# Performance work log

Measured on AMD Instinct MI355X. Metric: run time of the kernel, lower is better.

The kernel has to match this reference:

```python
import jax, jax.numpy as jnp
import numpy as np

D = 1024      # n_embd
F = 1024      # moe_inter_dim (ffn_hidden_size)
E = 8         # moe_num_experts
K = 2         # moe_top_k
B, T = 2, 2048


def setup_inputs() -> dict:
    key = jax.random.key(0)
    ks = jax.random.split(key, 7)
    std = 0.02
    x = jax.random.normal(ks[0], (B, T, D), dtype=jnp.float32)
    router_w = jax.random.normal(ks[1], (D, E), dtype=jnp.float32) * std
    w1 = jax.random.normal(ks[2], (E, D, F), dtype=jnp.float32) * std  # expert up proj
    w2 = jax.random.normal(ks[3], (E, F, D), dtype=jnp.float32) * std  # expert down proj
    shared_gate_up = jax.random.normal(ks[4], (D, 2 * F), dtype=jnp.float32) * std
    shared_down = jax.random.normal(ks[5], (F, D), dtype=jnp.float32) * std
    shared_gate_w = jax.random.normal(ks[6], (D, 1), dtype=jnp.float32) * std
    return {"x": x, "router_w": router_w, "w1": w1, "w2": w2,
            "shared_gate_up": shared_gate_up, "shared_down": shared_down,
            "shared_gate_w": shared_gate_w}


def _moe_forward(x, router_w, w1, w2, shared_gate_up, shared_down, shared_gate_w):
    b, t, d = x.shape
    xf = x.reshape(-1, d)                                   # [N, D]
    n = xf.shape[0]

    # --- router: softmax over experts, top-k scores used directly as combine weights ---
    logits = xf @ router_w                                  # [N, E]
    probs = jax.nn.softmax(logits, axis=-1)
    topw, topi = jax.lax.top_k(probs, K)                    # [N, K]
    combine = jnp.zeros((n, E), dtype=probs.dtype).at[
        jnp.arange(n)[:, None], topi].add(topw)             # [N, E] sparse combine weights

    # --- expert MLP: h = silu(x @ w1_e) @ w2_e, combined with routing weights ---
    h = jax.nn.silu(jnp.einsum('nd,edf->nef', xf, w1))      # [N, E, F]
    ye = jnp.einsum('nef,efd->ned', h, w2)                  # [N, E, D]
    routed = jnp.einsum('ne,ned->nd', combine, ye)          # [N, D]

    # --- shared expert SwiGLU, gated by sigmoid(x @ shared_gate_w) ---
    gu = xf @ shared_gate_up                                # [N, 2F]
    gate, up = gu[:, :F], gu[:, F:]
    shared = (jax.nn.silu(gate) * up) @ shared_down         # [N, D]
    shared = jax.nn.sigmoid(xf @ shared_gate_w) * shared

    return (routed + shared).reshape(b, t, d)


def reference(x, router_w, w1, w2, shared_gate_up, shared_down, shared_gate_w):
    return _moe_forward(x, router_w, w1, w2, shared_gate_up, shared_down, shared_gate_w)
```

## Files before the change

kernel.cpp:

```cpp
#include <hip/hip_runtime.h>
#include <math.h>

typedef __bf16 bf16_t;
typedef __bf16 bf16x8 __attribute__((ext_vector_type(8)));
typedef float f32x4 __attribute__((ext_vector_type(4)));

#define N_TOK 4096
#define DMODEL 1024
#define FFN 1024
#define NEXP 8
#define HIST_BLK 16

#define BM 128
#define BN 128
#define BK 32
#define LDK 40

__global__ void cvt_f32_to_bf16_kernel(const float* __restrict__ in, bf16_t* __restrict__ out, int n) {
  int i = (blockIdx.x * blockDim.x + threadIdx.x) * 8;
  if (i >= n) return;
  float4 a = *reinterpret_cast<const float4*>(in + i);
  float4 b = *reinterpret_cast<const float4*>(in + i + 4);
  bf16x8 o;
  o[0] = (bf16_t)a.x; o[1] = (bf16_t)a.y; o[2] = (bf16_t)a.z; o[3] = (bf16_t)a.w;
  o[4] = (bf16_t)b.x; o[5] = (bf16_t)b.y; o[6] = (bf16_t)b.z; o[7] = (bf16_t)b.w;
  *reinterpret_cast<bf16x8*>(out + i) = o;
}

__global__ void transpose_to_bf16_kernel(const float* __restrict__ in, bf16_t* __restrict__ out,
                                         int R, int C) {
  __shared__ float tile[32][33];
  size_t base = (size_t)blockIdx.z * R * C;
  int c0 = blockIdx.x * 32, r0 = blockIdx.y * 32;
  int tx = threadIdx.x, ty = threadIdx.y;
#pragma unroll
  for (int i = 0; i < 32; i += 8)
    tile[ty + i][tx] = in[base + (size_t)(r0 + ty + i) * C + (c0 + tx)];
  __syncthreads();
#pragma unroll
  for (int i = 0; i < 32; i += 8)
    out[base + (size_t)(c0 + ty + i) * R + (r0 + tx)] = (bf16_t)tile[tx][ty + i];
}

__global__ void router_kernel(const float* __restrict__ x, const float* __restrict__ rw,
                              const float* __restrict__ gw, int* __restrict__ topi,
                              float* __restrict__ topw, float* __restrict__ sig) {
  const int t = blockIdx.x;
  const int lane = threadIdx.x;
  const float* xr = x + (size_t)t * DMODEL;
  float acc[NEXP] = {0.f, 0.f, 0.f, 0.f, 0.f, 0.f, 0.f, 0.f};
  float accg = 0.f;
#pragma unroll 4
  for (int i = 0; i < DMODEL / 64; i++) {
    int d = i * 64 + lane;
    float xv = xr[d];
    const float4* r = reinterpret_cast<const float4*>(rw + (size_t)d * NEXP);
    float4 r0 = r[0], r1 = r[1];
    acc[0] += xv * r0.x; acc[1] += xv * r0.y; acc[2] += xv * r0.z; acc[3] += xv * r0.w;
    acc[4] += xv * r1.x; acc[5] += xv * r1.y; acc[6] += xv * r1.z; acc[7] += xv * r1.w;
    accg += xv * gw[d];
  }
#pragma unroll
  for (int e = 0; e < NEXP; e++)
    for (int s = 32; s > 0; s >>= 1) acc[e] += __shfl_down(acc[e], s, 64);
  for (int s = 32; s > 0; s >>= 1) accg += __shfl_down(accg, s, 64);
  if (lane == 0) {
    float mx = acc[0];
#pragma unroll
    for (int e = 1; e < NEXP; e++) mx = fmaxf(mx, acc[e]);
    float p[NEXP], sum = 0.f;
#pragma unroll
    for (int e = 0; e < NEXP; e++) { p[e] = __expf(acc[e] - mx); sum += p[e]; }
    int i1 = 0;
#pragma unroll
    for (int e = 1; e < NEXP; e++) if (acc[e] > acc[i1]) i1 = e;
    int i2 = (i1 == 0) ? 1 : 0;
#pragma unroll
    for (int e = 0; e < NEXP; e++) if (e != i1 && acc[e] > acc[i2]) i2 = e;
    float inv = 1.f / sum;
    topi[2 * t] = i1;     topw[2 * t] = p[i1] * inv;
    topi[2 * t + 1] = i2; topw[2 * t + 1] = p[i2] * inv;
    sig[t] = 1.f / (1.f + __expf(-accg));
  }
}

__global__ void hist_kernel(const int* __restrict__ topi, int* __restrict__ block_counts) {
  __shared__ int h[NEXP];
  const int tid = threadIdx.x;
  if (tid < NEXP) h[tid] = 0;
  __syncthreads();
  const int t = blockIdx.x * 256 + tid;
  atomicAdd(&h[topi[2 * t]], 1);
  atomicAdd(&h[topi[2 * t + 1]], 1);
  __syncthreads();
  if (tid < NEXP) block_counts[blockIdx.x * NEXP + tid] = h[tid];
}

__global__ void scan_kernel(const int* __restrict__ block_counts, int* __restrict__ offsets,
                            int* __restrict__ counts, int* __restrict__ block_base) {
  int o = 0;
  for (int e = 0; e < NEXP; e++) {
    int tot = 0;
    for (int b = 0; b < HIST_BLK; b++) {
      block_base[b * NEXP + e] = o + tot;
      tot += block_counts[b * NEXP + e];
    }
    offsets[e] = o;
    counts[e] = tot;
    o += tot;
  }
}

__global__ void gather_kernel(const int* __restrict__ topi, const float* __restrict__ topw,
                              const int* __restrict__ block_base, int* __restrict__ slot_tok,
                              float* __restrict__ slot_w, int* __restrict__ slot_of) {
  __shared__ int cur[NEXP];
  const int tid = threadIdx.x;
  if (tid < NEXP) cur[tid] = block_base[blockIdx.x * NEXP + tid];
  __syncthreads();
  const int t = blockIdx.x * 256 + tid;
#pragma unroll
  for (int j = 0; j < 2; j++) {
    int e = topi[2 * t + j];
    int s = atomicAdd(&cur[e], 1);
    slot_tok[s] = t;
    slot_w[s] = topw[2 * t + j];
    slot_of[2 * t + j] = s;
  }
}

__global__ void silu_mul_kernel(const bf16_t* __restrict__ GU, bf16_t* __restrict__ S) {
  int i = blockIdx.x * blockDim.x + threadIdx.x;
  int t = i >> 7;
  int f = (i & 127) << 3;
  const bf16_t* grp = GU + (size_t)t * (2 * FFN) + f;
  bf16x8 g = *reinterpret_cast<const bf16x8*>(grp);
  bf16x8 u = *reinterpret_cast<const bf16x8*>(grp + FFN);
  bf16x8 o;
#pragma unroll
  for (int j = 0; j < 8; j++) {
    float gv = (float)g[j], uv = (float)u[j];
    o[j] = (bf16_t)(gv / (1.f + __expf(-gv)) * uv);
  }
  *reinterpret_cast<bf16x8*>(S + (size_t)t * FFN + f) = o;
}

__global__ void combine_kernel(const bf16_t* __restrict__ Y, const int* __restrict__ slot_of,
                               float* __restrict__ out) {
  int i = blockIdx.x * blockDim.x + threadIdx.x;
  int t = i >> 7;
  int d = (i & 127) << 3;
  int s0 = slot_of[2 * t], s1 = slot_of[2 * t + 1];
  bf16x8 a = *reinterpret_cast<const bf16x8*>(Y + (size_t)s0 * DMODEL + d);
  bf16x8 b = *reinterpret_cast<const bf16x8*>(Y + (size_t)s1 * DMODEL + d);
  float* o = out + (size_t)t * DMODEL + d;
  float4 o0 = *reinterpret_cast<float4*>(o);
  float4 o1 = *reinterpret_cast<float4*>(o + 4);
  o0.x += (float)a[0] + (float)b[0]; o0.y += (float)a[1] + (float)b[1];
  o0.z += (float)a[2] + (float)b[2]; o0.w += (float)a[3] + (float)b[3];
  o1.x += (float)a[4] + (float)b[4]; o1.y += (float)a[5] + (float)b[5];
  o1.z += (float)a[6] + (float)b[6]; o1.w += (float)a[7] + (float)b[7];
  *reinterpret_cast<float4*>(o) = o0;
  *reinterpret_cast<float4*>(o + 4) = o1;
}

template <int MODE>
__global__ __launch_bounds__(256) void gemm_kernel(
    const bf16_t* __restrict__ A, const bf16_t* __restrict__ B, void* __restrict__ Cout,
    int N, int K, const int* __restrict__ offsets, const int* __restrict__ counts,
    const int* __restrict__ slot_tok, const float* __restrict__ slot_w,
    const float* __restrict__ sig) {
  __shared__ bf16_t lds_a[BM * LDK];
  __shared__ bf16_t lds_b[BN * LDK];

  const int e = blockIdx.z;
  int m0, mEnd;
  const bf16_t* Bp = B;
  if (MODE == 1 || MODE == 2) {
    const int off = offsets[e], cnt = counts[e];
    m0 = off + (int)blockIdx.y * BM;
    mEnd = off + cnt;
    if (m0 >= mEnd) return;
    Bp += (size_t)e * N * K;
  } else {
    m0 = blockIdx.y * BM;
    mEnd = N_TOK;
  }
  const int n0 = blockIdx.x * BN;

  const int tid = threadIdx.x;
  const int lane = tid & 63;
  const int wave = tid >> 6;
  const int wm = (wave >> 1) * 64;
  const int wn = (wave & 1) * 64;
  const int qd = lane >> 4;
  const int lm = lane & 15;

  const int arow = tid >> 2;
  const int cc = tid & 3;
  const bf16_t* pa[2];
  const bf16_t* pb[2];
#pragma unroll
  for (int h = 0; h < 2; h++) {
    int s = m0 + arow + h * 64;
    int g;
    if (MODE == 1) g = (s < mEnd) ? slot_tok[s] : 0;
    else if (MODE == 2) g = (s < mEnd) ? s : (mEnd - 1);
    else g = s;
    pa[h] = A + (size_t)g * K;
    pb[h] = Bp + (size_t)(n0 + arow + h * 64) * K;
  }

  f32x4 acc[4][4] = {};

  for (int k0 = 0; k0 < K; k0 += BK) {
    __syncthreads();
#pragma unroll
    for (int h = 0; h < 2; h++) {
      *reinterpret_cast<uint4*>(&lds_a[(arow + h * 64) * LDK + cc * 8]) =
          *reinterpret_cast<const uint4*>(pa[h] + k0 + cc * 8);
      *reinterpret_cast<uint4*>(&lds_b[(arow + h * 64) * LDK + cc * 8]) =
          *reinterpret_cast<const uint4*>(pb[h] + k0 + cc * 8);
    }
    __syncthreads();
    bf16x8 af[4], bfr[4];
#pragma unroll
    for (int i = 0; i < 4; i++)
      af[i] = *reinterpret_cast<const bf16x8*>(&lds_a[(wm + i * 16 + lm) * LDK + qd * 8]);
#pragma unroll
    for (int j = 0; j < 4; j++)
      bfr[j] = *reinterpret_cast<const bf16x8*>(&lds_b[(wn + j * 16 + lm) * LDK + qd * 8]);
#pragma unroll
    for (int i = 0; i < 4; i++)
#pragma unroll
      for (int j = 0; j < 4; j++)
        acc[i][j] = __builtin_amdgcn_mfma_f32_16x16x32_bf16(af[i], bfr[j], acc[i][j], 0, 0, 0);
  }

#pragma unroll
  for (int i = 0; i < 4; i++) {
#pragma unroll
    for (int r = 0; r < 4; r++) {
      const int gm = m0 + wm + i * 16 + qd * 4 + r;
      if ((MODE == 1 || MODE == 2) && gm >= mEnd) continue;
      const float wgt = (MODE == 2) ? slot_w[gm] : 0.f;
#pragma unroll
      for (int j = 0; j < 4; j++) {
        const int col = n0 + wn + j * 16 + lm;
        float v = acc[i][j][r];
        if (MODE == 0) {
          ((bf16_t*)Cout)[(size_t)gm * N + col] = (bf16_t)v;
        } else if (MODE == 1) {
          ((bf16_t*)Cout)[(size_t)gm * FFN + col] = (bf16_t)(v / (1.f + __expf(-v)));
        } else if (MODE == 2) {
          ((bf16_t*)Cout)[(size_t)gm * DMODEL + col] = (bf16_t)(wgt * v);
        } else {
          ((float*)Cout)[(size_t)gm * DMODEL + col] = sig[gm] * v;
        }
      }
    }
  }
}

extern "C" void kernel_launch(void* const* d_in, const int* in_sizes, int n_in, void* d_out,
                              int out_size, void* d_ws, size_t ws_size, hipStream_t stream) {
  const float* x = (const float*)d_in[0];
  const float* rw = (const float*)d_in[1];
  const float* w1 = (const float*)d_in[2];
  const float* w2 = (const float*)d_in[3];
  const float* sgu = (const float*)d_in[4];
  const float* sdw = (const float*)d_in[5];
  const float* gw = (const float*)d_in[6];
  float* out = (float*)d_out;

  char* ws = (char*)d_ws;
  size_t off = 0;
  auto alloc = [&](size_t bytes) -> void* {
    void* p = ws + off;
    off += (bytes + 255) & ~(size_t)255;
    return p;
  };
  bf16_t* xb = (bf16_t*)alloc((size_t)N_TOK * DMODEL * 2);
  bf16_t* w1t = (bf16_t*)alloc((size_t)NEXP * DMODEL * FFN * 2);
  bf16_t* w2t = (bf16_t*)alloc((size_t)NEXP * DMODEL * FFN * 2);
  bf16_t* sgut = (bf16_t*)alloc((size_t)2 * FFN * DMODEL * 2);
  bf16_t* sdt = (bf16_t*)alloc((size_t)DMODEL * FFN * 2);
  bf16_t* GU = (bf16_t*)alloc((size_t)N_TOK * 2 * FFN * 2);
  bf16_t* S = (bf16_t*)alloc((size_t)N_TOK * FFN * 2);
  bf16_t* Y = (bf16_t*)alloc((size_t)N_TOK * 2 * DMODEL * 2);
  int* topi = (int*)alloc(N_TOK * 2 * 4);
  float* topw = (float*)alloc(N_TOK * 2 * 4);
  float* sig = (float*)alloc(N_TOK * 4);
  int* slot_tok = (int*)alloc(N_TOK * 2 * 4);
  float* slot_w = (float*)alloc(N_TOK * 2 * 4);
  int* slot_of = (int*)alloc(N_TOK * 2 * 4);
  int* block_counts = (int*)alloc(HIST_BLK * NEXP * 4);
  int* block_base = (int*)alloc(HIST_BLK * NEXP * 4);
  int* counts = (int*)alloc(NEXP * 4);
  int* offsets = (int*)alloc(NEXP * 4);
  bf16_t* H = GU;

  cvt_f32_to_bf16_kernel<<<N_TOK * DMODEL / 8 / 256, 256, 0, stream>>>(x, xb, N_TOK * DMODEL);
  transpose_to_bf16_kernel<<<dim3(FFN / 32, DMODEL / 32, NEXP), dim3(32, 8), 0, stream>>>(
      w1, w1t, DMODEL, FFN);
  transpose_to_bf16_kernel<<<dim3(DMODEL / 32, FFN / 32, NEXP), dim3(32, 8), 0, stream>>>(
      w2, w2t, FFN, DMODEL);
  transpose_to_bf16_kernel<<<dim3(2 * FFN / 32, DMODEL / 32, 1), dim3(32, 8), 0, stream>>>(
      sgu, sgut, DMODEL, 2 * FFN);
  transpose_to_bf16_kernel<<<dim3(DMODEL / 32, FFN / 32, 1), dim3(32, 8), 0, stream>>>(
      sdw, sdt, FFN, DMODEL);

  router_kernel<<<N_TOK, 64, 0, stream>>>(x, rw, gw, topi, topw, sig);
  hist_kernel<<<HIST_BLK, 256, 0, stream>>>(topi, block_counts);
  scan_kernel<<<1, 1, 0, stream>>>(block_counts, offsets, counts, block_base);
  gather_kernel<<<HIST_BLK, 256, 0, stream>>>(topi, topw, block_base, slot_tok, slot_w, slot_of);

  gemm_kernel<0><<<dim3(2 * FFN / BN, N_TOK / BM, 1), 256, 0, stream>>>(
      xb, sgut, GU, 2 * FFN, DMODEL, nullptr, nullptr, nullptr, nullptr, nullptr);
  silu_mul_kernel<<<N_TOK * FFN / 8 / 256, 256, 0, stream>>>(GU, S);
  gemm_kernel<3><<<dim3(DMODEL / BN, N_TOK / BM, 1), 256, 0, stream>>>(
      S, sdt, out, DMODEL, FFN, nullptr, nullptr, nullptr, nullptr, sig);

  gemm_kernel<1><<<dim3(FFN / BN, N_TOK / BM, NEXP), 256, 0, stream>>>(
      xb, w1t, H, FFN, DMODEL, offsets, counts, slot_tok, nullptr, nullptr);
  gemm_kernel<2><<<dim3(DMODEL / BN, N_TOK / BM, NEXP), 256, 0, stream>>>(
      H, w2t, Y, DMODEL, FFN, offsets, counts, slot_tok, slot_w, nullptr);
  combine_kernel<<<N_TOK * DMODEL / 8 / 256, 256, 0, stream>>>(Y, slot_of, out);
}
```

Before: 320.7 us.

## Fuse shared and routed GEMMs, fold cast into router, use direct global-to-LDS loads

Merges the four weight-transpose launches into one kernel and folds the x-to-bf16 cast into the router kernel. The shared-expert gate/up columns are interleaved so SwiGLU is computed in the GEMM epilogue through a lane shuffle, which removes the silu_mul pass and the GU buffer. Shared and routed GEMMs now share one launch per phase along the z dimension, and tiles are staged with global_load_lds into unpadded LDS. This cuts launches and intermediate memory traffic, but dropping the LDS padding may bring bank conflicts, and half the lanes in the shared epilogue sit idle.

```diff
diff --git a/kernel.cpp b/kernel.cpp
--- a/kernel.cpp
+++ b/kernel.cpp
@@ -3,6 +3,7 @@
 
 typedef __bf16 bf16_t;
 typedef __bf16 bf16x8 __attribute__((ext_vector_type(8)));
+typedef __bf16 bf16x4 __attribute__((ext_vector_type(4)));
 typedef float f32x4 __attribute__((ext_vector_type(4)));
 
 #define N_TOK 4096
@@ -14,51 +15,72 @@
 #define BM 128
 #define BN 128
 #define BK 32
-#define LDK 40
-
-__global__ void cvt_f32_to_bf16_kernel(const float* __restrict__ in, bf16_t* __restrict__ out, int n) {
-  int i = (blockIdx.x * blockDim.x + threadIdx.x) * 8;
-  if (i >= n) return;
-  float4 a = *reinterpret_cast<const float4*>(in + i);
-  float4 b = *reinterpret_cast<const float4*>(in + i + 4);
-  bf16x8 o;
-  o[0] = (bf16_t)a.x; o[1] = (bf16_t)a.y; o[2] = (bf16_t)a.z; o[3] = (bf16_t)a.w;
-  o[4] = (bf16_t)b.x; o[5] = (bf16_t)b.y; o[6] = (bf16_t)b.z; o[7] = (bf16_t)b.w;
-  *reinterpret_cast<bf16x8*>(out + i) = o;
-}
-
-__global__ void transpose_to_bf16_kernel(const float* __restrict__ in, bf16_t* __restrict__ out,
-                                         int R, int C) {
+
+typedef __attribute__((address_space(3))) uint32_t lds_u32_t;
+typedef const __attribute__((address_space(1))) uint32_t glb_u32_t;
+
+__global__ void transpose_all_kernel(const float* __restrict__ w1, const float* __restrict__ w2,
+                                     const float* __restrict__ sgu, const float* __restrict__ sdw,
+                                     bf16_t* __restrict__ w1t, bf16_t* __restrict__ w2t,
+                                     bf16_t* __restrict__ sgut, bf16_t* __restrict__ sdt) {
   __shared__ float tile[32][33];
-  size_t base = (size_t)blockIdx.z * R * C;
-  int c0 = blockIdx.x * 32, r0 = blockIdx.y * 32;
-  int tx = threadIdx.x, ty = threadIdx.y;
+  const int z = blockIdx.z;
+  const float* in;
+  bf16_t* out;
+  int C = 1024;
+  bool remap = false;
+  if (z < 8) {
+    in = w1 + (size_t)z * 1048576; out = w1t + (size_t)z * 1048576;
+  } else if (z < 16) {
+    in = w2 + (size_t)(z - 8) * 1048576; out = w2t + (size_t)(z - 8) * 1048576;
+  } else if (z == 16) {
+    in = sgu; out = sgut; C = 2048; remap = true;
+  } else {
+    in = sdw; out = sdt;
+  }
+  const int R = 1024;
+  const int c0 = blockIdx.x * 32, r0 = blockIdx.y * 32;
+  if (c0 >= C) return;
+  const int tx = threadIdx.x, ty = threadIdx.y;
 #pragma unroll
   for (int i = 0; i < 32; i += 8)
-    tile[ty + i][tx] = in[base + (size_t)(r0 + ty + i) * C + (c0 + tx)];
+    tile[ty + i][tx] = in[(size_t)(r0 + ty + i) * C + (c0 + tx)];
   __syncthreads();
 #pragma unroll
-  for (int i = 0; i < 32; i += 8)
-    out[base + (size_t)(c0 + ty + i) * R + (r0 + tx)] = (bf16_t)tile[tx][ty + i];
+  for (int i = 0; i < 32; i += 8) {
+    int c = c0 + ty + i;
+    int oc = remap ? ((c < FFN) ? 2 * c : 2 * (c - FFN) + 1) : c;
+    out[(size_t)oc * R + (r0 + tx)] = (bf16_t)tile[tx][ty + i];
+  }
 }
 
 __global__ void router_kernel(const float* __restrict__ x, const float* __restrict__ rw,
-                              const float* __restrict__ gw, int* __restrict__ topi,
-                              float* __restrict__ topw, float* __restrict__ sig) {
+                              const float* __restrict__ gw, bf16_t* __restrict__ xb,
+                              int* __restrict__ topi, float* __restrict__ topw,
+                              float* __restrict__ sig) {
   const int t = blockIdx.x;
   const int lane = threadIdx.x;
   const float* xr = x + (size_t)t * DMODEL;
+  bf16_t* xbr = xb + (size_t)t * DMODEL;
   float acc[NEXP] = {0.f, 0.f, 0.f, 0.f, 0.f, 0.f, 0.f, 0.f};
   float accg = 0.f;
-#pragma unroll 4
-  for (int i = 0; i < DMODEL / 64; i++) {
-    int d = i * 64 + lane;
-    float xv = xr[d];
-    const float4* r = reinterpret_cast<const float4*>(rw + (size_t)d * NEXP);
-    float4 r0 = r[0], r1 = r[1];
-    acc[0] += xv * r0.x; acc[1] += xv * r0.y; acc[2] += xv * r0.z; acc[3] += xv * r0.w;
-    acc[4] += xv * r1.x; acc[5] += xv * r1.y; acc[6] += xv * r1.z; acc[7] += xv * r1.w;
-    accg += xv * gw[d];
+#pragma unroll
+  for (int i = 0; i < 4; i++) {
+    const int d = i * 256 + lane * 4;
+    float4 xv = *reinterpret_cast<const float4*>(xr + d);
+    bf16x4 o;
+    o[0] = (bf16_t)xv.x; o[1] = (bf16_t)xv.y; o[2] = (bf16_t)xv.z; o[3] = (bf16_t)xv.w;
+    *reinterpret_cast<bf16x4*>(xbr + d) = o;
+    const float xs[4] = {xv.x, xv.y, xv.z, xv.w};
+#pragma unroll
+    for (int j = 0; j < 4; j++) {
+      const float4* r = reinterpret_cast<const float4*>(rw + (size_t)(d + j) * NEXP);
+      float4 r0 = r[0], r1 = r[1];
+      float xj = xs[j];
+      acc[0] += xj * r0.x; acc[1] += xj * r0.y; acc[2] += xj * r0.z; acc[3] += xj * r0.w;
+      acc[4] += xj * r1.x; acc[5] += xj * r1.y; acc[6] += xj * r1.z; acc[7] += xj * r1.w;
+      accg += xj * gw[d + j];
+    }
   }
 #pragma unroll
   for (int e = 0; e < NEXP; e++)
@@ -127,22 +149,6 @@
     slot_w[s] = topw[2 * t + j];
     slot_of[2 * t + j] = s;
   }
-}
-
-__global__ void silu_mul_kernel(const bf16_t* __restrict__ GU, bf16_t* __restrict__ S) {
-  int i = blockIdx.x * blockDim.x + threadIdx.x;
-  int t = i >> 7;
-  int f = (i & 127) << 3;
-  const bf16_t* grp = GU + (size_t)t * (2 * FFN) + f;
-  bf16x8 g = *reinterpret_cast<const bf16x8*>(grp);
-  bf16x8 u = *reinterpret_cast<const bf16x8*>(grp + FFN);
-  bf16x8 o;
-#pragma unroll
-  for (int j = 0; j < 8; j++) {
-    float gv = (float)g[j], uv = (float)u[j];
-    o[j] = (bf16_t)(gv / (1.f + __expf(-gv)) * uv);
-  }
-  *reinterpret_cast<bf16x8*>(S + (size_t)t * FFN + f) = o;
 }
 
 __global__ void combine_kernel(const bf16_t* __restrict__ Y, const int* __restrict__ slot_of,
@@ -164,72 +170,77 @@
   *reinterpret_cast<float4*>(o + 4) = o1;
 }
 
-template <int MODE>
-__global__ __launch_bounds__(256) void gemm_kernel(
-    const bf16_t* __restrict__ A, const bf16_t* __restrict__ B, void* __restrict__ Cout,
-    int N, int K, const int* __restrict__ offsets, const int* __restrict__ counts,
+template <int PHASE>
+__global__ __launch_bounds__(256) void moe_gemm_kernel(
+    const bf16_t* __restrict__ A0, const bf16_t* __restrict__ B0,
+    const bf16_t* __restrict__ A1, const bf16_t* __restrict__ B1,
+    void* __restrict__ C0, void* __restrict__ C1,
+    const int* __restrict__ offsets, const int* __restrict__ counts,
     const int* __restrict__ slot_tok, const float* __restrict__ slot_w,
     const float* __restrict__ sig) {
-  __shared__ bf16_t lds_a[BM * LDK];
-  __shared__ bf16_t lds_b[BN * LDK];
-
-  const int e = blockIdx.z;
+  __shared__ bf16_t lds_a[BM * BK];
+  __shared__ bf16_t lds_b[BN * BK];
+
+  const int z = blockIdx.z;
   int m0, mEnd;
-  const bf16_t* Bp = B;
-  if (MODE == 1 || MODE == 2) {
-    const int off = offsets[e], cnt = counts[e];
-    m0 = off + (int)blockIdx.y * BM;
-    mEnd = off + cnt;
-    if (m0 >= mEnd) return;
-    Bp += (size_t)e * N * K;
-  } else {
+  const bf16_t *Ap, *Bp;
+  if (z == 0) {
     m0 = blockIdx.y * BM;
     mEnd = N_TOK;
+    Ap = A0; Bp = B0;
+  } else {
+    if (PHASE == 0 && blockIdx.x >= FFN / BN) return;
+    const int e = z - 1;
+    m0 = offsets[e] + (int)blockIdx.y * BM;
+    mEnd = offsets[e] + counts[e];
+    if (m0 >= mEnd) return;
+    Ap = A1; Bp = B1 + (size_t)e * FFN * DMODEL;
   }
   const int n0 = blockIdx.x * BN;
 
   const int tid = threadIdx.x;
   const int lane = tid & 63;
   const int wave = tid >> 6;
+  const int qd = lane >> 4;
+  const int lm = lane & 15;
   const int wm = (wave >> 1) * 64;
   const int wn = (wave & 1) * 64;
-  const int qd = lane >> 4;
-  const int lm = lane & 15;
-
-  const int arow = tid >> 2;
-  const int cc = tid & 3;
+
+  const int cc = lane & 3;
+  const int rr = lane >> 2;
   const bf16_t* pa[2];
   const bf16_t* pb[2];
 #pragma unroll
-  for (int h = 0; h < 2; h++) {
-    int s = m0 + arow + h * 64;
+  for (int i = 0; i < 2; i++) {
+    int r = wave * 32 + i * 16 + rr;
+    int s = m0 + r;
     int g;
-    if (MODE == 1) g = (s < mEnd) ? slot_tok[s] : 0;
-    else if (MODE == 2) g = (s < mEnd) ? s : (mEnd - 1);
-    else g = s;
-    pa[h] = A + (size_t)g * K;
-    pb[h] = Bp + (size_t)(n0 + arow + h * 64) * K;
+    if (z == 0) g = s;
+    else if (PHASE == 0) g = slot_tok[(s < mEnd) ? s : (mEnd - 1)];
+    else g = (s < mEnd) ? s : (mEnd - 1);
+    pa[i] = Ap + (size_t)g * 1024 + cc * 8;
+    pb[i] = Bp + (size_t)(n0 + r) * 1024 + cc * 8;
   }
 
   f32x4 acc[4][4] = {};
 
-  for (int k0 = 0; k0 < K; k0 += BK) {
+  for (int k0 = 0; k0 < 1024; k0 += BK) {
     __syncthreads();
 #pragma unroll
-    for (int h = 0; h < 2; h++) {
-      *reinterpret_cast<uint4*>(&lds_a[(arow + h * 64) * LDK + cc * 8]) =
-          *reinterpret_cast<const uint4*>(pa[h] + k0 + cc * 8);
-      *reinterpret_cast<uint4*>(&lds_b[(arow + h * 64) * LDK + cc * 8]) =
-          *reinterpret_cast<const uint4*>(pb[h] + k0 + cc * 8);
+    for (int i = 0; i < 2; i++) {
+      __builtin_amdgcn_global_load_lds((glb_u32_t*)(pa[i] + k0),
+                                       (lds_u32_t*)&lds_a[(wave * 32 + i * 16) * BK], 16, 0, 0);
+      __builtin_amdgcn_global_load_lds((glb_u32_t*)(pb[i] + k0),
+                                       (lds_u32_t*)&lds_b[(wave * 32 + i * 16) * BK], 16, 0, 0);
     }
     __syncthreads();
     bf16x8 af[4], bfr[4];
 #pragma unroll
     for (int i = 0; i < 4; i++)
-      af[i] = *reinterpret_cast<const bf16x8*>(&lds_a[(wm + i * 16 + lm) * LDK + qd * 8]);
+      af[i] = *reinterpret_cast<const bf16x8*>(&lds_a[(wm + i * 16 + lm) * BK + qd * 8]);
 #pragma unroll
     for (int j = 0; j < 4; j++)
-      bfr[j] = *reinterpret_cast<const bf16x8*>(&lds_b[(wn + j * 16 + lm) * LDK + qd * 8]);
+      bfr[j] = *reinterpret_cast<const bf16x8*>(&lds_b[(wn + j * 16 + lm) * BK + qd * 8]);
 #pragma unroll
     for (int i = 0; i < 4; i++)
 #pragma unroll
@@ -242,20 +253,27 @@
 #pragma unroll
     for (int r = 0; r < 4; r++) {
       const int gm = m0 + wm + i * 16 + qd * 4 + r;
-      if ((MODE == 1 || MODE == 2) && gm >= mEnd) continue;
-      const float wgt = (MODE == 2) ? slot_w[gm] : 0.f;
+      const bool mOk = (z == 0) || (gm < mEnd);
 #pragma unroll
       for (int j = 0; j < 4; j++) {
         const int col = n0 + wn + j * 16 + lm;
         float v = acc[i][j][r];
-        if (MODE == 0) {
-          ((bf16_t*)Cout)[(size_t)gm * N + col] = (bf16_t)v;
-        } else if (MODE == 1) {
-          ((bf16_t*)Cout)[(size_t)gm * FFN + col] = (bf16_t)(v / (1.f + __expf(-v)));
-        } else if (MODE == 2) {
-          ((bf16_t*)Cout)[(size_t)gm * DMODEL + col] = (bf16_t)(wgt * v);
+        if (PHASE == 0) {
+          if (z == 0) {
+            float u = __shfl_xor(v, 1, 64);
+            if ((lane & 1) == 0) {
+              float sv = v / (1.f + __expf(-v)) * u;
+              ((bf16_t*)C0)[(size_t)gm * FFN + (col >> 1)] = (bf16_t)sv;
+            }
+          } else if (mOk) {
+            ((bf16_t*)C1)[(size_t)gm * FFN + col] = (bf16_t)(v / (1.f + __expf(-v)));
+          }
         } else {
-          ((float*)Cout)[(size_t)gm * DMODEL + col] = sig[gm] * v;
+          if (z == 0) {
+            ((float*)C0)[(size_t)gm * DMODEL + col] = sig[gm] * v;
+          } else if (mOk) {
+            ((bf16_t*)C1)[(size_t)gm * DMODEL + col] = (bf16_t)(slot_w[gm] * v);
+          }
         }
       }
     }
@@ -285,8 +303,8 @@
   bf16_t* w2t = (bf16_t*)alloc((size_t)NEXP * DMODEL * FFN * 2);
   bf16_t* sgut = (bf16_t*)alloc((size_t)2 * FFN * DMODEL * 2);
   bf16_t* sdt = (bf16_t*)alloc((size_t)DMODEL * FFN * 2);
-  bf16_t* GU = (bf16_t*)alloc((size_t)N_TOK * 2 * FFN * 2);
   bf16_t* S = (bf16_t*)alloc((size_t)N_TOK * FFN * 2);
+  bf16_t* H = (bf16_t*)alloc((size_t)N_TOK * 2 * FFN * 2);
   bf16_t* Y = (bf16_t*)alloc((size_t)N_TOK * 2 * DMODEL * 2);
   int* topi = (int*)alloc(N_TOK * 2 * 4);
   float* topw = (float*)alloc(N_TOK * 2 * 4);
@@ -298,32 +316,17 @@
   int* block_base = (int*)alloc(HIST_BLK * NEXP * 4);
   int* counts = (int*)alloc(NEXP * 4);
   int* offsets = (int*)alloc(NEXP * 4);
-  bf16_t* H = GU;
-
-  cvt_f32_to_bf16_kernel<<<N_TOK * DMODEL / 8 / 256, 256, 0, stream>>>(x, xb, N_TOK * DMODEL);
-  transpose_to_bf16_kernel<<<dim3(FFN / 32, DMODEL / 32, NEXP), dim3(32, 8), 0, stream>>>(
-      w1, w1t, DMODEL, FFN);
-  transpose_to_bf16_kernel<<<dim3(DMODEL / 32, FFN / 32, NEXP), dim3(32, 8), 0, stream>>>(
-      w2, w2t, FFN, DMODEL);
-  transpose_to_bf16_kernel<<<dim3(2 * FFN / 32, DMODEL / 32, 1), dim3(32, 8), 0, stream>>>(
-      sgu, sgut, DMODEL, 2 * FFN);
-  transpose_to_bf16_kernel<<<dim3(DMODEL / 32, FFN / 32, 1), dim3(32, 8), 0, stream>>>(
-      sdw, sdt, FFN, DMODEL);
-
-  router_kernel<<<N_TOK, 64, 0, stream>>>(x, rw, gw, topi, topw, sig);
+
+  transpose_all_kernel<<<dim3(64, 32, 18), dim3(32, 8), 0, stream>>>(w1, w2, sgu, sdw, w1t, w2t,
+                                                                     sgut, sdt);
+  router_kernel<<<N_TOK, 64, 0, stream>>>(x, rw, gw, xb, topi, topw, sig);
   hist_kernel<<<HIST_BLK, 256, 0, stream>>>(topi, block_counts);
   scan_kernel<<<1, 1, 0, stream>>>(block_counts, offsets, counts, block_base);
   gather_kernel<<<HIST_BLK, 256, 0, stream>>>(topi, topw, block_base, slot_tok, slot_w, slot_of);
 
-  gemm_kernel<0><<<dim3(2 * FFN / BN, N_TOK / BM, 1), 256, 0, stream>>>(
-      xb, sgut, GU, 2 * FFN, DMODEL, nullptr, nullptr, nullptr, nullptr, nullptr);
-  silu_mul_kernel<<<N_TOK * FFN / 8 / 256, 256, 0, stream>>>(GU, S);
-  gemm_kernel<3><<<dim3(DMODEL / BN, N_TOK / BM, 1), 256, 0, stream>>>(
-      S, sdt, out, DMODEL, FFN, nullptr, nullptr, nullptr, nullptr, sig);
-
-  gemm_kernel<1><<<dim3(FFN / BN, N_TOK / BM, NEXP), 256, 0, stream>>>(
-      xb, w1t, H, FFN, DMODEL, offsets, counts, slot_tok, nullptr, nullptr);
-  gemm_kernel<2><<<dim3(DMODEL / BN, N_TOK / BM, NEXP), 256, 0, stream>>>(
-      H, w2t, Y, DMODEL, FFN, offsets, counts, slot_tok, slot_w, nullptr);
+  moe_gemm_kernel<0><<<dim3(2 * FFN / BN, N_TOK / BM, 1 + NEXP), 256, 0, stream>>>(
+      xb, sgut, xb, w1t, S, H, offsets, counts, slot_tok, slot_w, sig);
+  moe_gemm_kernel<1><<<dim3(DMODEL / BN, N_TOK / BM, 1 + NEXP), 256, 0, stream>>>(
+      S, sdt, H, w2t, out, Y, offsets, counts, slot_tok, slot_w, sig);
   combine_kernel<<<N_TOK * DMODEL / 8 / 256, 256, 0, stream>>>(Y, slot_of, out);
 }
```

New measurement: 326.1 us. About the same (+1.7%).
